# Optimization experiments

Hardware: AMD Instinct MI355X
Metric: run time of the kernel (lower is better)

The kernel has to match this reference:

```python
import jax, jax.numpy as jnp
import numpy as np

N = 50000       # nodes
E = 800000      # edges (avg degree 16)
C_IN = 128
C_OUT = 128
H = 4           # attention heads
D = C_OUT // H  # per-head dim
G = 8           # group-norm groups
NEG_SLOPE_ACT = 0.01   # nn.LeakyReLU() default
NEG_SLOPE_ATT = 0.2    # GAT attention LeakyReLU slope


def _glorot(key, shape):
    fan = shape[0] + (shape[-1] if len(shape) > 1 else shape[0])
    lim = np.sqrt(6.0 / fan).astype(np.float32)
    return jax.random.uniform(key, shape, jnp.float32, -lim, lim)


def setup_inputs() -> dict:
    key = jax.random.key(0)
    ks = jax.random.split(key, 8)
    inp = {
        "x": jax.random.normal(ks[0], (N, C_IN), jnp.float32),
        "edge_index": jax.random.randint(ks[1], (2, E), 0, N),
        "edge_weight": jax.random.uniform(ks[2], (E,), jnp.float32),
    }
    dims = [C_IN, C_OUT]
    for l in range(2):
        cin = dims[l]
        k = jax.random.split(ks[3 + l], 8)
        inp[f"gamma{l}"] = jnp.ones((cin,), jnp.float32)
        inp[f"beta{l}"] = jnp.zeros((cin,), jnp.float32)
        inp[f"W{l}"] = _glorot(k[0], (cin, H * D))
        inp[f"We{l}"] = _glorot(k[1], (1, H * D))
        inp[f"a_src{l}"] = _glorot(k[2], (H, D))
        inp[f"a_dst{l}"] = _glorot(k[3], (H, D))
        inp[f"a_edge{l}"] = _glorot(k[4], (H, D))
        inp[f"bias{l}"] = jnp.zeros((H * D,), jnp.float32)
    return inp


def group_norm(x, gamma, beta, eps=1e-5):
    n, c = x.shape
    xg = x.reshape(n, G, c // G)
    mu = xg.mean(-1, keepdims=True)
    var = xg.var(-1, keepdims=True)
    xn = ((xg - mu) * jax.lax.rsqrt(var + eps)).reshape(n, c)
    return xn * gamma + beta


def gat_layer(x, src, dst, ew, W, We, a_src, a_dst, a_edge, bias):
    h = (x @ W).reshape(N, H, D)                   # [N,H,D]
    he = (ew[:, None] @ We).reshape(-1, H, D)      # [E',H,D] edge-weight embedding
    logits = ((h * a_src).sum(-1)[src]
              + (h * a_dst).sum(-1)[dst]
              + (he * a_edge).sum(-1))             # [E',H]
    logits = jax.nn.leaky_relu(logits, NEG_SLOPE_ATT)
    m = jax.ops.segment_max(logits, dst, num_segments=N)
    m = jax.lax.stop_gradient(jnp.where(jnp.isfinite(m), m, 0.0))
    e = jnp.exp(logits - m[dst])
    s = jax.ops.segment_sum(e, dst, num_segments=N)
    alpha = e / (s[dst] + 1e-16)                   # softmax over in-edges per dst, per head
    out = jax.ops.segment_sum(alpha[:, :, None] * h[src], dst, num_segments=N)
    return out.reshape(N, H * D) + bias


def reference(x, edge_index, edge_weight,
              gamma0, beta0, W0, We0, a_src0, a_dst0, a_edge0, bias0,
              gamma1, beta1, W1, We1, a_src1, a_dst1, a_edge1, bias1):
    loop = jnp.arange(N)
    src = jnp.concatenate([edge_index[0], loop])
    dst = jnp.concatenate([edge_index[1], loop])
    # self-loop fill_value='max': self edges get the max edge weight
    ew = jnp.concatenate([edge_weight, jnp.full((N,), edge_weight.max())])
    params = [(gamma0, beta0, W0, We0, a_src0, a_dst0, a_edge0, bias0),
              (gamma1, beta1, W1, We1, a_src1, a_dst1, a_edge1, bias1)]
    for g, b, W, We, asrc, adst, ae, bias in params:
        x = group_norm(x, g, b)
        x = jax.nn.leaky_relu(x, NEG_SLOPE_ACT)
        x = gat_layer(x, src, dst, ew, W, We, asrc, adst, ae, bias)
    return x
```

## Files before the change

### kernel.cpp

```cpp
#include <hip/hip_runtime.h>
#include <hip/hip_bf16.h>
#include <math.h>

#define CN 128
#define NBLK 256
#define BSH 8

typedef __attribute__((ext_vector_type(8))) short bf16x8;
typedef __attribute__((ext_vector_type(4))) float f32x4;

static __device__ inline unsigned int pack_bf16x2(float lo, float hi) {
    unsigned int ul = __float_as_uint(lo);
    unsigned int uh = __float_as_uint(hi);
    ul = (ul + 0x7fffu + ((ul >> 16) & 1u)) >> 16;
    uh = (uh + 0x7fffu + ((uh >> 16) & 1u)) & 0xffff0000u;
    return ul | uh;
}
static __device__ inline unsigned short bf16_of(float v) {
    unsigned int u = __float_as_uint(v);
    return (unsigned short)((u + 0x7fffu + ((u >> 16) & 1u)) >> 16);
}

__global__ __launch_bounds__(256) void kbA(const int* __restrict__ dsts,
                                           const float* __restrict__ ew,
                                           int e, int n,
                                           int* __restrict__ hist,
                                           int* __restrict__ ewmaxArr,
                                           const float* __restrict__ W0,
                                           const float* __restrict__ W1,
                                           const float* __restrict__ We0,
                                           const float* __restrict__ ae0,
                                           const float* __restrict__ We1,
                                           const float* __restrict__ ae1,
                                           unsigned short* __restrict__ wt0,
                                           unsigned short* __restrict__ wt1,
                                           float* __restrict__ ce) {
    __shared__ int lh[256];
    __shared__ int wm[4];
    int t = threadIdx.x, blk = blockIdx.x;
    if (blk >= NBLK) {
        int b = blk - NBLK;
        if (b < 2) {
            const float* W = b ? W1 : W0;
            unsigned short* wt = b ? wt1 : wt0;
            for (int i = t; i < CN * CN; i += 256) {
                int k = i >> 7, c = i & 127;
                wt[c * CN + k] = bf16_of(W[k * CN + c]);
            }
        } else if (t < 8) {
            const float* We = (t < 4) ? We0 : We1;
            const float* ae = (t < 4) ? ae0 : ae1;
            int h = t & 3;
            float s = 0.f;
            for (int d = 0; d < 32; d++) s += We[h * 32 + d] * ae[h * 32 + d];
            ce[t] = s;
        }
        return;
    }
    lh[t] = 0;
    __syncthreads();
    int tot = e + n;
    int chunk = (tot + NBLK - 1) / NBLK;
    int start = blk * chunk, end = min(start + chunk, tot);
    float m = 0.f;
    for (int i = start + t; i < end; i += 256) {
        int d;
        if (i < e) { d = dsts[i]; m = fmaxf(m, ew[i]); }
        else       { d = i - e; }
        atomicAdd(&lh[d >> BSH], 1);
    }
#pragma unroll
    for (int off = 1; off < 64; off <<= 1) m = fmaxf(m, __shfl_xor(m, off));
    if ((t & 63) == 0) wm[t >> 6] = __float_as_int(m);
    __syncthreads();
    hist[t * NBLK + blk] = lh[t];
    if (t == 0)
        ewmaxArr[blk] = max(max(wm[0], wm[1]), max(wm[2], wm[3]));
}

__global__ __launch_bounds__(256) void kscanL(int* __restrict__ a,
                                              int* __restrict__ bsum) {
    __shared__ int wsum[4];
    int t = threadIdx.x, blk = blockIdx.x;
    int idx = blk * 256 + t;
    int v = a[idx];
    int s = v;
    int lane = t & 63, wid = t >> 6;
#pragma unroll
    for (int off = 1; off < 64; off <<= 1) {
        int u = __shfl_up(s, off);
        if (lane >= off) s += u;
    }
    if (lane == 63) wsum[wid] = s;
    __syncthreads();
    int add = 0;
#pragma unroll
    for (int w = 0; w < 4; w++) if (w < wid) add += wsum[w];
    s += add;
    a[idx] = s - v;
    if (t == 255) bsum[blk] = s;
}

__global__ __launch_bounds__(256) void kbB(const int* __restrict__ srcs,
                                           const int* __restrict__ dsts,
                                           const float* __restrict__ ew,
                                           const int* __restrict__ ewmaxArr,
                                           const int* __restrict__ hsc,
                                           const int* __restrict__ bsum,
                                           int2* __restrict__ inter, int e, int n) {
    __shared__ int cur[256];
    __shared__ int wsum[4];
    __shared__ int wmI;
    int t = threadIdx.x, blk = blockIdx.x;
    if (t == 0) wmI = 0;
    int v = bsum[t];
    int s = v;
    int lane = t & 63, wid = t >> 6;
#pragma unroll
    for (int off = 1; off < 64; off <<= 1) {
        int u = __shfl_up(s, off);
        if (lane >= off) s += u;
    }
    int mi = ewmaxArr[t];
#pragma unroll
    for (int off = 1; off < 64; off <<= 1) mi = max(mi, __shfl_xor(mi, off));
    if (lane == 63) wsum[wid] = s;
    __syncthreads();
    int add = 0;
#pragma unroll
    for (int w = 0; w < 4; w++) if (w < wid) add += wsum[w];
    s += add;
    cur[t] = hsc[t * NBLK + blk] + (s - v);
    if (lane == 0) atomicMax(&wmI, mi);
    __syncthreads();
    float wmax = __int_as_float(wmI);
    int tot = e + n;
    int chunk = (tot + NBLK - 1) / NBLK;
    int start = blk * chunk, end = min(start + chunk, tot);
    for (int i = start + t; i < end; i += 256) {
        int sn, d; float w;
        if (i < e) { sn = srcs[i]; d = dsts[i]; w = ew[i]; }
        else       { sn = i - e;   d = sn;      w = wmax;  }
        int p = atomicAdd(&cur[d >> BSH], 1);
        inter[p] = make_int2((d << 16) | sn, __float_as_int(w));
    }
}

static __device__ void kbc_body(int* cnt, int* cur, int* wsum, int* bexc,
                                int b,
                                const int* __restrict__ hsc,
                                const int* __restrict__ bsum,
                                const int2* __restrict__ inter,
                                unsigned int* __restrict__ edges,
                                int* __restrict__ rowptr,
                                int n, int nb, int ep) {
    int t = threadIdx.x;
    int lane = t & 63, wid = t >> 6;
    {
        int v = bsum[t];
        int s = v;
#pragma unroll
        for (int off = 1; off < 64; off <<= 1) {
            int u = __shfl_up(s, off);
            if (lane >= off) s += u;
        }
        if (lane == 63) wsum[wid] = s;
        __syncthreads();
        int add = 0;
#pragma unroll
        for (int w = 0; w < 4; w++) if (w < wid) add += wsum[w];
        s += add;
        bexc[t] = s - v;
        if (t == 255) bexc[256] = s;
    }
    cnt[t] = 0;
    __syncthreads();
    int rstart = hsc[b * NBLK] + bexc[b];
    int rend = (b + 1 < 256) ? (hsc[(b + 1) * NBLK] + bexc[b + 1]) : ep;
    for (int i = rstart + t; i < rend; i += 256)
        atomicAdd(&cnt[(inter[i].x >> 16) & 255], 1);
    __syncthreads();
    int v = cnt[t];
    int s = v;
#pragma unroll
    for (int off = 1; off < 64; off <<= 1) {
        int u = __shfl_up(s, off);
        if (lane >= off) s += u;
    }
    if (lane == 63) wsum[wid] = s;
    __syncthreads();
    int wexcl = 0;
#pragma unroll
    for (int w = 0; w < 4; w++) if (w < wid) wexcl += wsum[w];
    int excl = wexcl + s - v;
    int node = (b << BSH) + t;
    int gpos = rstart + excl;
    if (node < n) rowptr[node] = gpos;
    if (b == nb - 1 && t == 0) rowptr[n] = ep;
    cur[t] = gpos;
    __syncthreads();
    for (int i = rstart + t; i < rend; i += 256) {
        int2 r = inter[i];
        int p = atomicAdd(&cur[(r.x >> 16) & 255], 1);
        unsigned int wb = bf16_of(__int_as_float(r.y));
        edges[p] = (unsigned int)(r.x & 0xffff) | (wb << 16);
    }
}

static __device__ void kgn_body(short* xs, short* ws, int block_row,
                                const float* __restrict__ xin,
                                const uint4* __restrict__ xin_b,
                                int inbf16, const float* __restrict__ gamma,
                                const float* __restrict__ beta,
                                const unsigned short* __restrict__ wt,
                                const float* __restrict__ asrc,
                                const float* __restrict__ adst,
                                unsigned int* __restrict__ hout,
                                float* __restrict__ ssrc,
                                float* __restrict__ sdst, int n) {
    int t = threadIdx.x;
    int lane = t & 63, w = t >> 6;
    int m = lane & 15, quad = lane >> 4;

    {
        const uint4* src = (const uint4*)wt;
        uint4* dst = (uint4*)ws;
#pragma unroll
        for (int i = 0; i < 8; i++) {
            int u = t + 256 * i;
            int c = u >> 4, kb = u & 15;
            dst[c * 16 + (kb ^ (c & 15))] = src[u];
        }
    }
    {
        int r = t & 63;
        int row = block_row + r;
        uint4* dst = (uint4*)xs;
#pragma unroll
        for (int u2 = 0; u2 < 2; u2++) {
            int g = (t >> 6) * 2 + u2;
            uint4 lo, hi;
            if (row < n) {
                float v[16];
                if (inbf16) {
                    uint4 A = xin_b[(size_t)row * 16 + g * 2];
                    uint4 B = xin_b[(size_t)row * 16 + g * 2 + 1];
                    unsigned int uu[8] = {A.x,A.y,A.z,A.w,B.x,B.y,B.z,B.w};
#pragma unroll
                    for (int j = 0; j < 8; j++) {
                        v[2*j]   = __uint_as_float(uu[j] << 16);
                        v[2*j+1] = __uint_as_float(uu[j] & 0xffff0000u);
                    }
                } else {
                    const float4* xr = (const float4*)(xin + (size_t)row * CN + g * 16);
                    float4 A = xr[0], B = xr[1], C = xr[2], D = xr[3];
                    float tmp[16] = {A.x,A.y,A.z,A.w,B.x,B.y,B.z,B.w,
                                     C.x,C.y,C.z,C.w,D.x,D.y,D.z,D.w};
#pragma unroll
                    for (int j = 0; j < 16; j++) v[j] = tmp[j];
                }
                float mu = 0.f;
#pragma unroll
                for (int j = 0; j < 16; j++) mu += v[j];
                mu *= 0.0625f;
                float var = 0.f;
#pragma unroll
                for (int j = 0; j < 16; j++) { float d2 = v[j] - mu; var += d2 * d2; }
                var *= 0.0625f;
                float rsv = rsqrtf(var + 1e-5f);
                const float4* gp = (const float4*)(gamma + g * 16);
                const float4* bp = (const float4*)(beta + g * 16);
                float4 g0 = gp[0], g1 = gp[1], g2 = gp[2], g3 = gp[3];
                float4 b0 = bp[0], b1 = bp[1], b2 = bp[2], b3 = bp[3];
                float gv[16] = {g0.x,g0.y,g0.z,g0.w,g1.x,g1.y,g1.z,g1.w,
                                g2.x,g2.y,g2.z,g2.w,g3.x,g3.y,g3.z,g3.w};
                float bv[16] = {b0.x,b0.y,b0.z,b0.w,b1.x,b1.y,b1.z,b1.w,
                                b2.x,b2.y,b2.z,b2.w,b3.x,b3.y,b3.z,b3.w};
                float xn[16];
#pragma unroll
                for (int j = 0; j < 16; j++) {
                    float xv = (v[j] - mu) * rsv * gv[j] + bv[j];
                    xn[j] = xv > 0.f ? xv : 0.01f * xv;
                }
                lo = make_uint4(pack_bf16x2(xn[0], xn[1]),  pack_bf16x2(xn[2], xn[3]),
                                pack_bf16x2(xn[4], xn[5]),  pack_bf16x2(xn[6], xn[7]));
                hi = make_uint4(pack_bf16x2(xn[8], xn[9]),  pack_bf16x2(xn[10], xn[11]),
                                pack_bf16x2(xn[12], xn[13]), pack_bf16x2(xn[14], xn[15]));
            } else {
                lo = make_uint4(0, 0, 0, 0);
                hi = lo;
            }
            dst[r * 16 + ((2 * g)     ^ (r & 15))] = lo;
            dst[r * 16 + ((2 * g + 1) ^ (r & 15))] = hi;
        }
    }
    __syncthreads();

    f32x4 acc[4][2];
#pragma unroll
    for (int i = 0; i < 4; i++) { acc[i][0] = (f32x4)0.f; acc[i][1] = (f32x4)0.f; }

#pragma unroll
    for (int kc = 0; kc < 4; kc++) {
        int kb = 4 * kc + quad;
        bf16x8 af[4], bfr[2];
#pragma unroll
        for (int mt = 0; mt < 4; mt++)
            af[mt] = *(const bf16x8*)&xs[(16 * mt + m) * CN + ((kb ^ m) << 3)];
#pragma unroll
        for (int nt = 0; nt < 2; nt++) {
            int c = 32 * w + 16 * nt + m;
            bfr[nt] = *(const bf16x8*)&ws[c * CN + ((kb ^ m) << 3)];
        }
#pragma unroll
        for (int mt = 0; mt < 4; mt++) {
#pragma unroll
            for (int nt = 0; nt < 2; nt++)
                acc[mt][nt] = __builtin_amdgcn_mfma_f32_16x16x32_bf16(
                    af[mt], bfr[nt], acc[mt][nt], 0, 0, 0);
        }
    }

    float asv[2], adv[2];
#pragma unroll
    for (int nt = 0; nt < 2; nt++) {
        asv[nt] = asrc[32 * w + 16 * nt + m];
        adv[nt] = adst[32 * w + 16 * nt + m];
    }
#pragma unroll
    for (int mt = 0; mt < 4; mt++) {
#pragma unroll
        for (int j = 0; j < 4; j++) {
            float p = acc[mt][0][j] * asv[0] + acc[mt][1][j] * asv[1];
            float q = acc[mt][0][j] * adv[0] + acc[mt][1][j] * adv[1];
#pragma unroll
            for (int off = 1; off < 16; off <<= 1) {
                p += __shfl_xor(p, off);
                q += __shfl_xor(q, off);
            }
            if (m == 0) {
                int row = block_row + 16 * mt + 4 * quad + j;
                if (row < n) {
                    ssrc[row * 4 + w] = p;
                    sdst[row * 4 + w] = q;
                }
            }
        }
    }

    __syncthreads();
#pragma unroll
    for (int mt = 0; mt < 4; mt++) {
#pragma unroll
        for (int nt = 0; nt < 2; nt++) {
            int c = 32 * w + 16 * nt + m;
#pragma unroll
            for (int j = 0; j < 4; j++) {
                int rl = 16 * mt + 4 * quad + j;
                xs[rl * CN + c] = (short)bf16_of(acc[mt][nt][j]);
            }
        }
    }
    __syncthreads();
    {
        const uint4* src = (const uint4*)xs;
#pragma unroll
        for (int i = 0; i < 4; i++) {
            int u = t + 256 * i;
            int rl = u >> 4;
            int row = block_row + rl;
            if (row < n)
                *(uint4*)&hout[(size_t)row * 64 + ((u & 15) << 2)] = src[u];
        }
    }
}

__global__ __launch_bounds__(256, 3) void kbCgn(
        const int* __restrict__ hsc, const int* __restrict__ bsum,
        const int2* __restrict__ inter, unsigned int* __restrict__ edges,
        int* __restrict__ rowptr, int n, int nb, int ep,
        const float* __restrict__ xin, const float* __restrict__ gamma,
        const float* __restrict__ beta, const unsigned short* __restrict__ wt,
        const float* __restrict__ asrc, const float* __restrict__ adst,
        unsigned int* __restrict__ hout, float* __restrict__ ssrcO,
        float* __restrict__ sdstO) {
    __shared__ short xs[64 * CN];
    __shared__ short ws[CN * CN];
    if ((int)blockIdx.x < nb) {
        int* cnt  = (int*)xs;
        int* cur  = (int*)(xs + 512);
        int* wsum = (int*)(xs + 1024);
        int* bexc = (int*)(xs + 2048);
        kbc_body(cnt, cur, wsum, bexc, blockIdx.x,
                 hsc, bsum, inter, edges, rowptr, n, nb, ep);
        return;
    }
    kgn_body(xs, ws, ((int)blockIdx.x - nb) * 64, xin, (const uint4*)0, 0,
             gamma, beta, wt, asrc, adst, hout, ssrcO, sdstO, n);
}

__global__ __launch_bounds__(256, 3) void kgn_gemm7(
        const float* __restrict__ xin, const uint4* __restrict__ xin_b,
        int inbf16, const float* __restrict__ gamma,
        const float* __restrict__ beta, const unsigned short* __restrict__ wt,
        const float* __restrict__ asrc, const float* __restrict__ adst,
        unsigned int* __restrict__ hout, float* __restrict__ ssrc,
        float* __restrict__ sdst, int n) {
    __shared__ short xs[64 * CN];
    __shared__ short ws[CN * CN];
    kgn_body(xs, ws, blockIdx.x * 64, xin, xin_b, inbf16,
             gamma, beta, wt, asrc, adst, hout, ssrc, sdst, n);
}

__global__ __launch_bounds__(256, 8) void kaggr3(
        const uint4* __restrict__ h, const float* __restrict__ ssrc,
        const float* __restrict__ sdst, const int* __restrict__ rowptr,
        const unsigned int* __restrict__ edges, const float* __restrict__ ce4,
        const float* __restrict__ bias, float* __restrict__ out,
        uint4* __restrict__ outb, int packout, int n) {
    int t = threadIdx.x;
    int node = blockIdx.x * 4 + (t >> 6);
    if (node >= n) return;
    int l64 = t & 63;
    int ll = l64 & 15;
    int g  = l64 >> 4;
    int head = ll >> 2;

    int start = rowptr[node], end = rowptr[node + 1];
    float sd = sdst[node * 4 + head];
    float ce = ce4[head];

    float a0=0.f,a1=0.f,a2=0.f,a3=0.f,a4=0.f,a5=0.f,a6=0.f,a7=0.f;
    float se = 0.f;

    int i = start + g;
    for (; i + 12 < end; i += 16) {
        unsigned int er[4];
#pragma unroll
        for (int u = 0; u < 4; u++) er[u] = edges[i + 4 * u];
        float ssv[4]; uint4 U[4];
#pragma unroll
        for (int u = 0; u < 4; u++) {
            int sidx = er[u] & 0xffff;
            ssv[u] = ssrc[sidx * 4 + head];
            U[u] = h[(size_t)sidx * 16 + ll];
        }
#pragma unroll
        for (int u = 0; u < 4; u++) {
            float wv = __uint_as_float(er[u] & 0xffff0000u);
            float l = ssv[u] + sd + wv * ce;
            l = fmaxf(l, 0.2f * l);
            float e = __expf(fminf(l, 80.f));
            float h0 = __uint_as_float(U[u].x << 16);
            float h1 = __uint_as_float(U[u].x & 0xffff0000u);
            float h2 = __uint_as_float(U[u].y << 16);
            float h3 = __uint_as_float(U[u].y & 0xffff0000u);
            float h4 = __uint_as_float(U[u].z << 16);
            float h5 = __uint_as_float(U[u].z & 0xffff0000u);
            float h6 = __uint_as_float(U[u].w << 16);
            float h7 = __uint_as_float(U[u].w & 0xffff0000u);
            se += e;
            a0 = fmaf(e, h0, a0); a1 = fmaf(e, h1, a1);
            a2 = fmaf(e, h2, a2); a3 = fmaf(e, h3, a3);
            a4 = fmaf(e, h4, a4); a5 = fmaf(e, h5, a5);
            a6 = fmaf(e, h6, a6); a7 = fmaf(e, h7, a7);
        }
    }
    for (; i < end; i += 4) {
        unsigned int er = edges[i];
        int sidx = er & 0xffff;
        float ss = ssrc[sidx * 4 + head];
        uint4 U = h[(size_t)sidx * 16 + ll];
        float wv = __uint_as_float(er & 0xffff0000u);
        float l = ss + sd + wv * ce;
        l = fmaxf(l, 0.2f * l);
        float e = __expf(fminf(l, 80.f));
        float h0 = __uint_as_float(U.x << 16);
        float h1 = __uint_as_float(U.x & 0xffff0000u);
        float h2 = __uint_as_float(U.y << 16);
        float h3 = __uint_as_float(U.y & 0xffff0000u);
        float h4 = __uint_as_float(U.z << 16);
        float h5 = __uint_as_float(U.z & 0xffff0000u);
        float h6 = __uint_as_float(U.w << 16);
        float h7 = __uint_as_float(U.w & 0xffff0000u);
        se += e;
        a0 = fmaf(e, h0, a0); a1 = fmaf(e, h1, a1);
        a2 = fmaf(e, h2, a2); a3 = fmaf(e, h3, a3);
        a4 = fmaf(e, h4, a4); a5 = fmaf(e, h5, a5);
        a6 = fmaf(e, h6, a6); a7 = fmaf(e, h7, a7);
    }
#pragma unroll
    for (int off = 16; off < 64; off <<= 1) {
        a0 += __shfl_xor(a0, off); a1 += __shfl_xor(a1, off);
        a2 += __shfl_xor(a2, off); a3 += __shfl_xor(a3, off);
        a4 += __shfl_xor(a4, off); a5 += __shfl_xor(a5, off);
        a6 += __shfl_xor(a6, off); a7 += __shfl_xor(a7, off);
        se += __shfl_xor(se, off);
    }
    if (g == 0) {
        float inv = 1.f / (se + 1e-16f);
        const float4* bp = (const float4*)(bias + ll * 8);
        float4 b0 = bp[0], b1 = bp[1];
        float o0 = a0 * inv + b0.x, o1 = a1 * inv + b0.y;
        float o2 = a2 * inv + b0.z, o3 = a3 * inv + b0.w;
        float o4 = a4 * inv + b1.x, o5 = a5 * inv + b1.y;
        float o6 = a6 * inv + b1.z, o7 = a7 * inv + b1.w;
        if (packout) {
            outb[(size_t)node * 16 + ll] =
                make_uint4(pack_bf16x2(o0, o1), pack_bf16x2(o2, o3),
                           pack_bf16x2(o4, o5), pack_bf16x2(o6, o7));
        } else {
            float4* orow = (float4*)(out + (size_t)node * CN + ll * 8);
            orow[0] = make_float4(o0, o1, o2, o3);
            orow[1] = make_float4(o4, o5, o6, o7);
        }
    }
}

extern "C" void kernel_launch(void* const* d_in, const int* in_sizes, int n_in,
                              void* d_out, int out_size, void* d_ws, size_t ws_size,
                              hipStream_t stream) {
    const float* x  = (const float*)d_in[0];
    const int*   ei = (const int*)d_in[1];
    const float* ew = (const float*)d_in[2];
    int N_ = in_sizes[0] / CN;
    int E_ = in_sizes[2];
    int EP = E_ + N_;
    int NB = (N_ + 255) >> BSH;
    int NT = (N_ + 63) / 64;

    size_t off = 0;
    auto alloc = [&](size_t bytes) -> void* {
        void* p = (char*)d_ws + off;
        off += (bytes + 255) & ~(size_t)255;
        return p;
    };
    unsigned int* hbuf = (unsigned int*)alloc((size_t)N_ * 64 * 4);
    uint4* x1b     = (uint4*)alloc((size_t)N_ * 64 * 4);
    float* ssrc    = (float*)alloc((size_t)N_ * 4 * 4);
    float* sdst    = (float*)alloc((size_t)N_ * 4 * 4);
    int*   rowptr  = (int*)alloc((size_t)(N_ + 1) * 4);
    unsigned int* edges = (unsigned int*)alloc((size_t)EP * 4);
    int2*  inter   = (int2*)alloc((size_t)EP * 8);
    int*   hist    = (int*)alloc((size_t)256 * NBLK * 4);
    int*   bsum    = (int*)alloc(1024);
    int*   ewmaxArr= (int*)alloc((size_t)NBLK * 4);
    unsigned short* wt0 = (unsigned short*)alloc((size_t)CN * CN * 2);
    unsigned short* wt1 = (unsigned short*)alloc((size_t)CN * CN * 2);
    float* cedge   = (float*)alloc(256);

    const int* srcs = ei;
    const int* dsts = ei + E_;

    kbA<<<NBLK + 3, 256, 0, stream>>>(dsts, ew, E_, N_, hist, ewmaxArr,
                                      (const float*)d_in[5], (const float*)d_in[13],
                                      (const float*)d_in[6], (const float*)d_in[9],
                                      (const float*)d_in[14], (const float*)d_in[17],
                                      wt0, wt1, cedge);
    kscanL<<<256, 256, 0, stream>>>(hist, bsum);
    kbB<<<NBLK, 256, 0, stream>>>(srcs, dsts, ew, ewmaxArr, hist, bsum, inter, E_, N_);

    kbCgn<<<NB + NT, 256, 0, stream>>>(
        hist, bsum, inter, edges, rowptr, N_, NB, EP,
        x, (const float*)d_in[3], (const float*)d_in[4], wt0,
        (const float*)d_in[7], (const float*)d_in[8],
        hbuf, ssrc, sdst);

    kaggr3<<<(N_ + 3) / 4, 256, 0, stream>>>(
        (const uint4*)hbuf, ssrc, sdst, rowptr, edges, cedge,
        (const float*)d_in[10], (float*)d_out, x1b, 1, N_);

    kgn_gemm7<<<NT, 256, 0, stream>>>(
        x, (const uint4*)x1b, 1, (const float*)d_in[11], (const float*)d_in[12],
        wt1, (const float*)d_in[15], (const float*)d_in[16],
        hbuf, ssrc, sdst, N_);
    kaggr3<<<(N_ + 3) / 4, 256, 0, stream>>>(
        (const uint4*)hbuf, ssrc, sdst, rowptr, edges, cedge + 4,
        (const float*)d_in[18], (float*)d_out, x1b, 0, N_);
}
```

Before: 256.9 us.

## Split aggregation into alpha precompute and head-partitioned gather passes

Replaces the fused per-node aggregation kernel with two kernels. The first computes normalized attention coefficients per edge and head and stores them as fp16. The second gathers features from a head-partitioned copy of h, written by the GEMM as four planes of 32 channels, so each gather pass touches only a quarter of the feature table and may keep it in cache. This adds an extra kernel launch and alpha traffic per layer, and lowers the precision of the attention weights.

```diff
diff --git a/kernel.cpp b/kernel.cpp
--- a/kernel.cpp
+++ b/kernel.cpp
@@ -1,5 +1,6 @@
 #include <hip/hip_runtime.h>
 #include <hip/hip_bf16.h>
+#include <hip/hip_fp16.h>
 #include <math.h>
 
 #define CN 128
@@ -215,9 +216,9 @@
                                 const unsigned short* __restrict__ wt,
                                 const float* __restrict__ asrc,
                                 const float* __restrict__ adst,
-                                unsigned int* __restrict__ hout,
+                                uint4* __restrict__ hout,
                                 float* __restrict__ ssrc,
-                                float* __restrict__ sdst, int n) {
+                                float* __restrict__ sdst, int n, int nstride) {
     int t = threadIdx.x;
     int lane = t & 63, w = t >> 6;
     int m = lane & 15, quad = lane >> 4;
@@ -369,8 +370,10 @@
             int u = t + 256 * i;
             int rl = u >> 4;
             int row = block_row + rl;
+            int chunk = u & 15;
+            int p = chunk >> 2, q = chunk & 3;
             if (row < n)
-                *(uint4*)&hout[(size_t)row * 64 + ((u & 15) << 2)] = src[u];
+                hout[((size_t)p * nstride + row) * 4 + q] = src[u];
         }
     }
 }
@@ -382,8 +385,8 @@
         const float* __restrict__ xin, const float* __restrict__ gamma,
         const float* __restrict__ beta, const unsigned short* __restrict__ wt,
         const float* __restrict__ asrc, const float* __restrict__ adst,
-        unsigned int* __restrict__ hout, float* __restrict__ ssrcO,
-        float* __restrict__ sdstO) {
+        uint4* __restrict__ hout, float* __restrict__ ssrcO,
+        float* __restrict__ sdstO, int nstride) {
     __shared__ short xs[64 * CN];
     __shared__ short ws[CN * CN];
     if ((int)blockIdx.x < nb) {
@@ -396,7 +399,7 @@
         return;
     }
     kgn_body(xs, ws, ((int)blockIdx.x - nb) * 64, xin, (const uint4*)0, 0,
-             gamma, beta, wt, asrc, adst, hout, ssrcO, sdstO, n);
+             gamma, beta, wt, asrc, adst, hout, ssrcO, sdstO, n, nstride);
 }
 
 __global__ __launch_bounds__(256, 3) void kgn_gemm7(
@@ -404,53 +407,98 @@
         int inbf16, const float* __restrict__ gamma,
         const float* __restrict__ beta, const unsigned short* __restrict__ wt,
         const float* __restrict__ asrc, const float* __restrict__ adst,
-        unsigned int* __restrict__ hout, float* __restrict__ ssrc,
-        float* __restrict__ sdst, int n) {
+        uint4* __restrict__ hout, float* __restrict__ ssrc,
+        float* __restrict__ sdst, int n, int nstride) {
     __shared__ short xs[64 * CN];
     __shared__ short ws[CN * CN];
     kgn_body(xs, ws, blockIdx.x * 64, xin, xin_b, inbf16,
-             gamma, beta, wt, asrc, adst, hout, ssrc, sdst, n);
-}
-
-__global__ __launch_bounds__(256, 8) void kaggr3(
-        const uint4* __restrict__ h, const float* __restrict__ ssrc,
-        const float* __restrict__ sdst, const int* __restrict__ rowptr,
-        const unsigned int* __restrict__ edges, const float* __restrict__ ce4,
-        const float* __restrict__ bias, float* __restrict__ out,
-        uint4* __restrict__ outb, int packout, int n) {
+             gamma, beta, wt, asrc, adst, hout, ssrc, sdst, n, nstride);
+}
+
+__global__ __launch_bounds__(256, 8) void kalpha(
+        const float* __restrict__ ssrc, const float* __restrict__ sdst,
+        const int* __restrict__ rowptr, const unsigned int* __restrict__ edges,
+        const float* __restrict__ ce4, __half* __restrict__ alpha,
+        int ep, int n) {
     int t = threadIdx.x;
     int node = blockIdx.x * 4 + (t >> 6);
     if (node >= n) return;
-    int l64 = t & 63;
-    int ll = l64 & 15;
-    int g  = l64 >> 4;
-    int head = ll >> 2;
-
+    int l = t & 63;
     int start = rowptr[node], end = rowptr[node + 1];
-    float sd = sdst[node * 4 + head];
-    float ce = ce4[head];
+    float4 sd = *(const float4*)&sdst[node * 4];
+    float4 ce = *(const float4*)ce4;
+
+    float se0 = 0.f, se1 = 0.f, se2 = 0.f, se3 = 0.f;
+    for (int i = start + l; i < end; i += 64) {
+        unsigned int er = edges[i];
+        int s = er & 0xffff;
+        float w = __uint_as_float(er & 0xffff0000u);
+        float4 ss = *(const float4*)&ssrc[s * 4];
+        float l0 = ss.x + sd.x + w * ce.x; l0 = fmaxf(l0, 0.2f * l0);
+        float l1 = ss.y + sd.y + w * ce.y; l1 = fmaxf(l1, 0.2f * l1);
+        float l2 = ss.z + sd.z + w * ce.z; l2 = fmaxf(l2, 0.2f * l2);
+        float l3 = ss.w + sd.w + w * ce.w; l3 = fmaxf(l3, 0.2f * l3);
+        se0 += __expf(fminf(l0, 80.f));
+        se1 += __expf(fminf(l1, 80.f));
+        se2 += __expf(fminf(l2, 80.f));
+        se3 += __expf(fminf(l3, 80.f));
+    }
+#pragma unroll
+    for (int off = 1; off < 64; off <<= 1) {
+        se0 += __shfl_xor(se0, off); se1 += __shfl_xor(se1, off);
+        se2 += __shfl_xor(se2, off); se3 += __shfl_xor(se3, off);
+    }
+    float i0 = 1.f / (se0 + 1e-16f), i1 = 1.f / (se1 + 1e-16f);
+    float i2 = 1.f / (se2 + 1e-16f), i3 = 1.f / (se3 + 1e-16f);
+    for (int i = start + l; i < end; i += 64) {
+        unsigned int er = edges[i];
+        int s = er & 0xffff;
+        float w = __uint_as_float(er & 0xffff0000u);
+        float4 ss = *(const float4*)&ssrc[s * 4];
+        float l0 = ss.x + sd.x + w * ce.x; l0 = fmaxf(l0, 0.2f * l0);
+        float l1 = ss.y + sd.y + w * ce.y; l1 = fmaxf(l1, 0.2f * l1);
+        float l2 = ss.z + sd.z + w * ce.z; l2 = fmaxf(l2, 0.2f * l2);
+        float l3 = ss.w + sd.w + w * ce.w; l3 = fmaxf(l3, 0.2f * l3);
+        alpha[i]            = __float2half(__expf(fminf(l0, 80.f)) * i0);
+        alpha[ep + i]       = __float2half(__expf(fminf(l1, 80.f)) * i1);
+        alpha[2 * ep + i]   = __float2half(__expf(fminf(l2, 80.f)) * i2);
+        alpha[3 * ep + i]   = __float2half(__expf(fminf(l3, 80.f)) * i3);
+    }
+}
+
+__global__ __launch_bounds__(256, 8) void kgather(
+        const uint4* __restrict__ hq, const __half* __restrict__ alpha,
+        const int* __restrict__ rowptr, const unsigned int* __restrict__ edges,
+        const float* __restrict__ bias, float* __restrict__ out,
+        uint4* __restrict__ outb, int packout, int ep, int n, int nstride,
+        int nbn) {
+    int blk = blockIdx.x;
+    int p = blk / nbn;
+    int node = (blk - p * nbn) * 4 + (threadIdx.x >> 6);
+    if (node >= n) return;
+    int l64 = threadIdx.x & 63;
+    int ll = l64 & 3;
+    int g  = l64 >> 2;
+
+    int start = rowptr[node], end = rowptr[node + 1];
+    const __half* ap = alpha + (size_t)p * ep;
+    const uint4*  hp = hq + (size_t)p * nstride * 4;
 
     float a0=0.f,a1=0.f,a2=0.f,a3=0.f,a4=0.f,a5=0.f,a6=0.f,a7=0.f;
-    float se = 0.f;
 
     int i = start + g;
-    for (; i + 12 < end; i += 16) {
-        unsigned int er[4];
-#pragma unroll
-        for (int u = 0; u < 4; u++) er[u] = edges[i + 4 * u];
-        float ssv[4]; uint4 U[4];
+    for (; i + 48 < end; i += 64) {
+        unsigned int er[4]; float av[4]; uint4 U[4];
+#pragma unroll
+        for (int u = 0; u < 4; u++) er[u] = edges[i + 16 * u];
 #pragma unroll
         for (int u = 0; u < 4; u++) {
-            int sidx = er[u] & 0xffff;
-            ssv[u] = ssrc[sidx * 4 + head];
-            U[u] = h[(size_t)sidx * 16 + ll];
+            av[u] = __half2float(ap[i + 16 * u]);
+            U[u] = hp[(size_t)(er[u] & 0xffff) * 4 + ll];
         }
 #pragma unroll
         for (int u = 0; u < 4; u++) {
-            float wv = __uint_as_float(er[u] & 0xffff0000u);
-            float l = ssv[u] + sd + wv * ce;
-            l = fmaxf(l, 0.2f * l);
-            float e = __expf(fminf(l, 80.f));
+            float e = av[u];
             float h0 = __uint_as_float(U[u].x << 16);
             float h1 = __uint_as_float(U[u].x & 0xffff0000u);
             float h2 = __uint_as_float(U[u].y << 16);
@@ -459,22 +507,16 @@
             float h5 = __uint_as_float(U[u].z & 0xffff0000u);
             float h6 = __uint_as_float(U[u].w << 16);
             float h7 = __uint_as_float(U[u].w & 0xffff0000u);
-            se += e;
             a0 = fmaf(e, h0, a0); a1 = fmaf(e, h1, a1);
             a2 = fmaf(e, h2, a2); a3 = fmaf(e, h3, a3);
             a4 = fmaf(e, h4, a4); a5 = fmaf(e, h5, a5);
             a6 = fmaf(e, h6, a6); a7 = fmaf(e, h7, a7);
         }
     }
-    for (; i < end; i += 4) {
+    for (; i < end; i += 16) {
         unsigned int er = edges[i];
-        int sidx = er & 0xffff;
-        float ss = ssrc[sidx * 4 + head];
-        uint4 U = h[(size_t)sidx * 16 + ll];
-        float wv = __uint_as_float(er & 0xffff0000u);
-        float l = ss + sd + wv * ce;
-        l = fmaxf(l, 0.2f * l);
-        float e = __expf(fminf(l, 80.f));
+        float e = __half2float(ap[i]);
+        uint4 U = hp[(size_t)(er & 0xffff) * 4 + ll];
         float h0 = __uint_as_float(U.x << 16);
         float h1 = __uint_as_float(U.x & 0xffff0000u);
         float h2 = __uint_as_float(U.y << 16);
@@ -483,34 +525,29 @@
         float h5 = __uint_as_float(U.z & 0xffff0000u);
         float h6 = __uint_as_float(U.w << 16);
         float h7 = __uint_as_float(U.w & 0xffff0000u);
-        se += e;
         a0 = fmaf(e, h0, a0); a1 = fmaf(e, h1, a1);
         a2 = fmaf(e, h2, a2); a3 = fmaf(e, h3, a3);
         a4 = fmaf(e, h4, a4); a5 = fmaf(e, h5, a5);
         a6 = fmaf(e, h6, a6); a7 = fmaf(e, h7, a7);
     }
 #pragma unroll
-    for (int off = 16; off < 64; off <<= 1) {
+    for (int off = 4; off < 64; off <<= 1) {
         a0 += __shfl_xor(a0, off); a1 += __shfl_xor(a1, off);
         a2 += __shfl_xor(a2, off); a3 += __shfl_xor(a3, off);
         a4 += __shfl_xor(a4, off); a5 += __shfl_xor(a5, off);
         a6 += __shfl_xor(a6, off); a7 += __shfl_xor(a7, off);
-        se += __shfl_xor(se, off);
     }
     if (g == 0) {
-        float inv = 1.f / (se + 1e-16f);
-        const float4* bp = (const float4*)(bias + ll * 8);
+        const float4* bp = (const float4*)(bias + p * 32 + ll * 8);
         float4 b0 = bp[0], b1 = bp[1];
-        float o0 = a0 * inv + b0.x, o1 = a1 * inv + b0.y;
-        float o2 = a2 * inv + b0.z, o3 = a3 * inv + b0.w;
-        float o4 = a4 * inv + b1.x, o5 = a5 * inv + b1.y;
-        float o6 = a6 * inv + b1.z, o7 = a7 * inv + b1.w;
+        float o0 = a0 + b0.x, o1 = a1 + b0.y, o2 = a2 + b0.z, o3 = a3 + b0.w;
+        float o4 = a4 + b1.x, o5 = a5 + b1.y, o6 = a6 + b1.z, o7 = a7 + b1.w;
         if (packout) {
-            outb[(size_t)node * 16 + ll] =
+            outb[(size_t)node * 16 + p * 4 + ll] =
                 make_uint4(pack_bf16x2(o0, o1), pack_bf16x2(o2, o3),
                            pack_bf16x2(o4, o5), pack_bf16x2(o6, o7));
         } else {
-            float4* orow = (float4*)(out + (size_t)node * CN + ll * 8);
+            float4* orow = (float4*)(out + (size_t)node * CN + p * 32 + ll * 8);
             orow[0] = make_float4(o0, o1, o2, o3);
             orow[1] = make_float4(o4, o5, o6, o7);
         }
@@ -528,6 +565,7 @@
     int EP = E_ + N_;
     int NB = (N_ + 255) >> BSH;
     int NT = (N_ + 63) / 64;
+    int NBn = (N_ + 3) / 4;
 
     size_t off = 0;
     auto alloc = [&](size_t bytes) -> void* {
@@ -535,12 +573,13 @@
         off += (bytes + 255) & ~(size_t)255;
         return p;
     };
-    unsigned int* hbuf = (unsigned int*)alloc((size_t)N_ * 64 * 4);
+    uint4* hbuf    = (uint4*)alloc((size_t)N_ * 64 * 4);
     uint4* x1b     = (uint4*)alloc((size_t)N_ * 64 * 4);
     float* ssrc    = (float*)alloc((size_t)N_ * 4 * 4);
     float* sdst    = (float*)alloc((size_t)N_ * 4 * 4);
     int*   rowptr  = (int*)alloc((size_t)(N_ + 1) * 4);
     unsigned int* edges = (unsigned int*)alloc((size_t)EP * 4);
+    __half* alphaB = (__half*)alloc((size_t)EP * 4 * 2);
     int2*  inter   = (int2*)alloc((size_t)EP * 8);
     int*   hist    = (int*)alloc((size_t)256 * NBLK * 4);
     int*   bsum    = (int*)alloc(1024);
@@ -564,17 +603,21 @@
         hist, bsum, inter, edges, rowptr, N_, NB, EP,
         x, (const float*)d_in[3], (const float*)d_in[4], wt0,
         (const float*)d_in[7], (const float*)d_in[8],
-        hbuf, ssrc, sdst);
-
-    kaggr3<<<(N_ + 3) / 4, 256, 0, stream>>>(
-        (const uint4*)hbuf, ssrc, sdst, rowptr, edges, cedge,
-        (const float*)d_in[10], (float*)d_out, x1b, 1, N_);
+        hbuf, ssrc, sdst, N_);
+
+    kalpha<<<NBn, 256, 0, stream>>>(ssrc, sdst, rowptr, edges, cedge,
+                                    alphaB, EP, N_);
+    kgather<<<4 * NBn, 256, 0, stream>>>(
+        hbuf, alphaB, rowptr, edges, (const float*)d_in[10],
+        (float*)d_out, x1b, 1, EP, N_, N_, NBn);
 
     kgn_gemm7<<<NT, 256, 0, stream>>>(
         x, (const uint4*)x1b, 1, (const float*)d_in[11], (const float*)d_in[12],
         wt1, (const float*)d_in[15], (const float*)d_in[16],
-        hbuf, ssrc, sdst, N_);
-    kaggr3<<<(N_ + 3) / 4, 256, 0, stream>>>(
-        (const uint4*)hbuf, ssrc, sdst, rowptr, edges, cedge + 4,
-        (const float*)d_in[18], (float*)d_out, x1b, 0, N_);
-}
+        hbuf, ssrc, sdst, N_, N_);
+    kalpha<<<NBn, 256, 0, stream>>>(ssrc, sdst, rowptr, edges, cedge + 4,
+                                    alphaB, EP, N_);
+    kgather<<<4 * NBn, 256, 0, stream>>>(
+        hbuf, alphaB, rowptr, edges, (const float*)d_in[18],
+        (float*)d_out, x1b, 0, EP, N_, N_, NBn);
+}
```

New measurement: 369.7 us. 1.44x slower.
